# Optimization experiments

Measured on AMD Instinct MI355X. Metric: run time of the kernel, lower is better.

## Reference

```python
import jax, jax.numpy as jnp
import numpy as np

N_NODES = 10000
N_EDGES = 320000
IN_FEATS = 512
OUT_FEATS = 64


def gcn(feat, src, dst, W, b):
    """DGL GraphConv with norm='both', allow_zero_in_degree=True.
    out = D_in^{-1/2} * A^T * (D_out^{-1/2} * feat) @ W + b  (degrees clamped to >=1).
    """
    ones_e = jnp.ones(src.shape[0], dtype=feat.dtype)
    deg_out = jnp.clip(jax.ops.segment_sum(ones_e, src, num_segments=N_NODES), 1.0)
    deg_in = jnp.clip(jax.ops.segment_sum(ones_e, dst, num_segments=N_NODES), 1.0)
    h = feat * jax.lax.rsqrt(deg_out)[:, None]          # [N, F_in]
    h = h @ W                                            # [N, F_out] (project first, F_in >= F_out)
    agg = jax.ops.segment_sum(h[src], dst, num_segments=N_NODES)  # [N, F_out]
    return agg * jax.lax.rsqrt(deg_in)[:, None] + b


def setup_inputs() -> dict:
    key = jax.random.key(0)
    ks = jax.random.split(key, 8)
    feat = jax.random.normal(ks[0], (N_NODES, IN_FEATS), dtype=jnp.float32)
    eps = jax.random.normal(ks[1], (N_NODES, OUT_FEATS), dtype=jnp.float32)
    src = jax.random.randint(ks[2], (N_EDGES,), 0, N_NODES, dtype=jnp.int32)
    dst = jax.random.randint(ks[3], (N_EDGES,), 0, N_NODES, dtype=jnp.int32)
    s1 = 1.0 / np.sqrt(IN_FEATS)
    s2 = 1.0 / np.sqrt(OUT_FEATS)
    W1 = jax.random.normal(ks[4], (IN_FEATS, OUT_FEATS), dtype=jnp.float32) * s1
    Wmu = jax.random.normal(ks[5], (OUT_FEATS, OUT_FEATS), dtype=jnp.float32) * s2
    Wstd = jax.random.normal(ks[6], (OUT_FEATS, OUT_FEATS), dtype=jnp.float32) * s2 - 2.0 * s2
    b1 = jnp.zeros((OUT_FEATS,), dtype=jnp.float32)
    bmu = jnp.zeros((OUT_FEATS,), dtype=jnp.float32)
    bstd = jnp.zeros((OUT_FEATS,), dtype=jnp.float32)
    return {"feat": feat, "eps": eps, "src": src, "dst": dst,
            "W1": W1, "b1": b1, "Wmu": Wmu, "bmu": bmu, "Wstd": Wstd, "bstd": bstd}


def reference(feat, eps, src, dst, W1, b1, Wmu, bmu, Wstd, bstd):
    h1 = gcn(feat, src, dst, W1, b1)            # [N, out]
    mu = gcn(h1, src, dst, Wmu, bmu)            # [N, out]
    logvar = gcn(h1, src, dst, Wstd, bstd)      # [N, out]
    std = jnp.exp(logvar)                       # logvar.exp_() is in-place in torch
    z = eps * std + mu                          # reparametrize
    adj = jax.nn.sigmoid(z @ z.T)               # [N, N] dense decode
    return adj, mu, std                         # torch returns mutated logvar (== std)
```

## Files before the change

### kernel.cpp

```cpp
#include <hip/hip_runtime.h>
#include <stdint.h>

#define N_NODES 10000
#define N_EDGES 320000
#define F_IN 512
#define F_OUT 64

typedef __attribute__((ext_vector_type(8)))  __bf16 bf16x8;
typedef __attribute__((ext_vector_type(8)))  short  short8;
typedef __attribute__((ext_vector_type(16))) float  f32x16;
typedef __attribute__((ext_vector_type(4)))  float  float4v;

#define OFF_H1P    0
#define OFF_H1     640000
#define OFF_MUP    1280000
#define OFF_STDP   1920000
#define OFF_DEGIN  2560000
#define OFF_DEGOUT 2570000
#define OFF_OFFS   2580000
#define OFF_CURS   2592000
#define OFF_SCIN   2604000
#define OFF_SCOUT  2616000
#define OFF_CSR    2628000
#define OFF_WBUF   2948000

__device__ __forceinline__ unsigned short f2bf(float f) {
    unsigned u = __builtin_bit_cast(unsigned, f);
    u += 0x7fffu + ((u >> 16) & 1u);
    return (unsigned short)(u >> 16);
}
__device__ __forceinline__ float bf2f(unsigned short h) {
    unsigned u = ((unsigned)h) << 16;
    return __builtin_bit_cast(float, u);
}
__device__ __forceinline__ f32x16 zero16() {
    f32x16 v;
#pragma unroll
    for (int i = 0; i < 16; ++i) v[i] = 0.f;
    return v;
}

__global__ void k0_deg_wswz(const int* __restrict__ src, const int* __restrict__ dst,
                            const float* __restrict__ W1,
                            int* __restrict__ deg_out, int* __restrict__ deg_in,
                            unsigned short* __restrict__ wbuf) {
    int bid = blockIdx.x, tid = threadIdx.x;
    if (bid < 1250) {
        int e = bid * 256 + tid;
        if (e < N_EDGES) {
            atomicAdd(&deg_out[src[e]], 1);
            atomicAdd(&deg_in[dst[e]], 1);
        }
    } else {
        int q = (bid - 1250) * 256 + tid;
        int j = q & 7, l = (q >> 3) & 63, c = (q >> 9) & 31, t = q >> 14;
        int k = c * 16 + ((l >> 5) << 3) + j;
        int n = (t << 5) + (l & 31);
        wbuf[q] = f2bf(W1[k * F_OUT + n]);
    }
}

__global__ void __launch_bounds__(1024) k1_scan(const int* __restrict__ deg_in,
                                                const int* __restrict__ deg_out,
                                                int* __restrict__ offs, int* __restrict__ curs,
                                                float* __restrict__ sc_in, float* __restrict__ sc_out) {
    __shared__ int sdata[1024];
    int t = threadIdx.x;
    int loc[10];
    int s = 0;
#pragma unroll
    for (int u = 0; u < 10; ++u) {
        int idx = t * 10 + u;
        int v = (idx < N_NODES) ? deg_in[idx] : 0;
        loc[u] = v; s += v;
    }
    sdata[t] = s;
    __syncthreads();
    for (int off = 1; off < 1024; off <<= 1) {
        int v = sdata[t];
        int add = (t >= off) ? sdata[t - off] : 0;
        __syncthreads();
        sdata[t] = v + add;
        __syncthreads();
    }
    int run = (t == 0) ? 0 : sdata[t - 1];
#pragma unroll
    for (int u = 0; u < 10; ++u) {
        int idx = t * 10 + u;
        if (idx < N_NODES) {
            offs[idx] = run; curs[idx] = run;
            run += loc[u];
            sc_in[idx] = rsqrtf((float)max(loc[u], 1));
            sc_out[idx] = rsqrtf((float)max(deg_out[idx], 1));
        }
    }
    if (t == 1023) offs[N_NODES] = sdata[1023];
}

__global__ void k2_csr(const int* __restrict__ src, const int* __restrict__ dst,
                       int* __restrict__ curs, int* __restrict__ csr) {
    int e = blockIdx.x * 256 + threadIdx.x;
    if (e < N_EDGES) {
        int d = dst[e];
        int p = atomicAdd(&curs[d], 1);
        csr[p] = src[e];
    }
}

__global__ void __launch_bounds__(256) k3_proj1(const float* __restrict__ feat,
                                                const unsigned short* __restrict__ wbuf,
                                                const float* __restrict__ sc_out,
                                                float* __restrict__ h1p) {
    __shared__ float red[4][32 * 64];
    int tid = threadIdx.x;
    int wid = tid >> 6;
    int l = tid & 63;
    int half = l >> 5;
    int rowbase = blockIdx.x * 32;
    int m = rowbase + (l & 31);
    if (m > N_NODES - 1) m = N_NODES - 1;
    const float* arow = feat + (size_t)m * F_IN + half * 8;

    f32x16 acc0 = zero16(), acc1 = zero16();
    int cbeg = wid * 8;
#pragma unroll
    for (int cc = 0; cc < 8; ++cc) {
        int c = cbeg + cc;
        float4v a0 = *(const float4v*)(arow + c * 16);
        float4v a1 = *(const float4v*)(arow + c * 16 + 4);
        short8 as;
        as[0] = (short)f2bf(a0[0]); as[1] = (short)f2bf(a0[1]);
        as[2] = (short)f2bf(a0[2]); as[3] = (short)f2bf(a0[3]);
        as[4] = (short)f2bf(a1[0]); as[5] = (short)f2bf(a1[1]);
        as[6] = (short)f2bf(a1[2]); as[7] = (short)f2bf(a1[3]);
        bf16x8 af = __builtin_bit_cast(bf16x8, as);
        bf16x8 b0 = __builtin_bit_cast(bf16x8, *(const short8*)(wbuf + (size_t)((0 * 32 + c) * 64 + l) * 8));
        bf16x8 b1 = __builtin_bit_cast(bf16x8, *(const short8*)(wbuf + (size_t)((1 * 32 + c) * 64 + l) * 8));
        acc0 = __builtin_amdgcn_mfma_f32_32x32x16_bf16(af, b0, acc0, 0, 0, 0);
        acc1 = __builtin_amdgcn_mfma_f32_32x32x16_bf16(af, b1, acc1, 0, 0, 0);
    }
#pragma unroll
    for (int r = 0; r < 16; ++r) {
        int row = (r & 3) + 8 * (r >> 2) + 4 * half;
        int col = l & 31;
        red[wid][row * 64 + col] = acc0[r];
        red[wid][row * 64 + 32 + col] = acc1[r];
    }
    __syncthreads();
#pragma unroll
    for (int i = 0; i < 8; ++i) {
        int idx = tid * 8 + i;
        int row = idx >> 6, col = idx & 63;
        int gr = rowbase + row;
        if (gr < N_NODES) {
            float v = red[0][idx] + red[1][idx] + red[2][idx] + red[3][idx];
            h1p[gr * F_OUT + col] = v * sc_out[gr];
        }
    }
}

__global__ void __launch_bounds__(256) k4_gather1(const int* __restrict__ offs, const int* __restrict__ csr,
                                                  const float* __restrict__ h1p, const float* __restrict__ sc_in,
                                                  const float* __restrict__ b1, float* __restrict__ h1) {
    int tid = threadIdx.x;
    int n = blockIdx.x * 4 + (tid >> 6);
    int o = tid & 63;
    int e0 = offs[n], e1 = offs[n + 1];
    float acc = 0.f;
    for (int e = e0; e < e1; ++e) {
        int s = csr[e];
        acc += h1p[s * F_OUT + o];
    }
    h1[n * F_OUT + o] = acc * sc_in[n] + b1[o];
}

__global__ void __launch_bounds__(256) k5_proj2(const float* __restrict__ h1,
                                                const float* __restrict__ Wmu, const float* __restrict__ Wstd,
                                                const float* __restrict__ sc_out,
                                                float* __restrict__ mup, float* __restrict__ stdp) {
    __shared__ float wmuT[64 * 65];
    __shared__ float wstdT[64 * 65];
    __shared__ float hrow[4 * 64];
    int tid = threadIdx.x;
    for (int i = tid; i < 4096; i += 256) {
        int k = i >> 6, o2 = i & 63;
        wmuT[o2 * 65 + k] = Wmu[i];
        wstdT[o2 * 65 + k] = Wstd[i];
    }
    int ln = tid >> 6, o = tid & 63;
    int n = blockIdx.x * 4 + ln;
    hrow[ln * 64 + o] = h1[n * F_OUT + o];
    __syncthreads();
    float amu = 0.f, asd = 0.f;
#pragma unroll
    for (int k = 0; k < 64; ++k) {
        float h = hrow[ln * 64 + k];
        amu += h * wmuT[o * 65 + k];
        asd += h * wstdT[o * 65 + k];
    }
    float s = sc_out[n];
    mup[n * F_OUT + o] = amu * s;
    stdp[n * F_OUT + o] = asd * s;
}

__global__ void __launch_bounds__(256) k6_gather2(const int* __restrict__ offs, const int* __restrict__ csr,
                                                  const float* __restrict__ mup, const float* __restrict__ stdp,
                                                  const float* __restrict__ sc_in,
                                                  const float* __restrict__ bmu, const float* __restrict__ bstd,
                                                  const float* __restrict__ eps,
                                                  float* __restrict__ out_mu, float* __restrict__ out_std,
                                                  unsigned short* __restrict__ zhi, unsigned short* __restrict__ zlo) {
    int tid = threadIdx.x;
    int n = blockIdx.x * 4 + (tid >> 6);
    int o = tid & 63;
    int e0 = offs[n], e1 = offs[n + 1];
    float amu = 0.f, alv = 0.f;
    for (int e = e0; e < e1; ++e) {
        int s = csr[e];
        amu += mup[s * F_OUT + o];
        alv += stdp[s * F_OUT + o];
    }
    float si = sc_in[n];
    float mu = amu * si + bmu[o];
    float lv = alv * si + bstd[o];
    float sd = __expf(lv);
    float z = eps[n * F_OUT + o] * sd + mu;
    out_mu[n * F_OUT + o] = mu;
    out_std[n * F_OUT + o] = sd;
    unsigned short h = f2bf(z);
    zhi[n * F_OUT + o] = h;
    zlo[n * F_OUT + o] = f2bf(z - bf2f(h));
}

#define NT_TILES 157
#define NT_CB    40
__global__ void __launch_bounds__(256) k7_adj(const unsigned short* __restrict__ zhi,
                                              const unsigned short* __restrict__ zlo,
                                              float* __restrict__ adj) {
    int bid = blockIdx.x;
    int xcd = bid & 7;
    int i = bid >> 3;
    int cb = i % NT_CB;
    int sti = xcd + 8 * (i / NT_CB);
    if (sti >= NT_TILES) return;

    int tid = threadIdx.x;
    int wid = tid >> 6, l = tid & 63;
    int stj = cb * 4 + wid;
    bool do_store = (stj < NT_TILES);
    if (stj >= NT_TILES) stj = NT_TILES - 1;

    int rbase = sti * 64, cbase = stj * 64;
    int half = l >> 5, lm = l & 31;
    int koff = half * 8;

    int ra0 = min(rbase + lm, N_NODES - 1);
    int ra1 = min(rbase + 32 + lm, N_NODES - 1);
    int rb0 = min(cbase + lm, N_NODES - 1);
    int rb1 = min(cbase + 32 + lm, N_NODES - 1);

    f32x16 acc[2][2];
    acc[0][0] = zero16(); acc[0][1] = zero16();
    acc[1][0] = zero16(); acc[1][1] = zero16();

#pragma unroll
    for (int c = 0; c < 4; ++c) {
        int ko = c * 16 + koff;
        bf16x8 ah[2], al[2], bh[2], bl[2];
        ah[0] = __builtin_bit_cast(bf16x8, *(const short8*)(zhi + (size_t)ra0 * 64 + ko));
        ah[1] = __builtin_bit_cast(bf16x8, *(const short8*)(zhi + (size_t)ra1 * 64 + ko));
        al[0] = __builtin_bit_cast(bf16x8, *(const short8*)(zlo + (size_t)ra0 * 64 + ko));
        al[1] = __builtin_bit_cast(bf16x8, *(const short8*)(zlo + (size_t)ra1 * 64 + ko));
        bh[0] = __builtin_bit_cast(bf16x8, *(const short8*)(zhi + (size_t)rb0 * 64 + ko));
        bh[1] = __builtin_bit_cast(bf16x8, *(const short8*)(zhi + (size_t)rb1 * 64 + ko));
        bl[0] = __builtin_bit_cast(bf16x8, *(const short8*)(zlo + (size_t)rb0 * 64 + ko));
        bl[1] = __builtin_bit_cast(bf16x8, *(const short8*)(zlo + (size_t)rb1 * 64 + ko));
#pragma unroll
        for (int rt = 0; rt < 2; ++rt)
#pragma unroll
            for (int ct = 0; ct < 2; ++ct) {
                acc[rt][ct] = __builtin_amdgcn_mfma_f32_32x32x16_bf16(ah[rt], bh[ct], acc[rt][ct], 0, 0, 0);
                acc[rt][ct] = __builtin_amdgcn_mfma_f32_32x32x16_bf16(ah[rt], bl[ct], acc[rt][ct], 0, 0, 0);
                acc[rt][ct] = __builtin_amdgcn_mfma_f32_32x32x16_bf16(al[rt], bh[ct], acc[rt][ct], 0, 0, 0);
            }
    }

#pragma unroll
    for (int rt = 0; rt < 2; ++rt)
#pragma unroll
        for (int ct = 0; ct < 2; ++ct) {
#pragma unroll
            for (int r = 0; r < 16; ++r) {
                int row = rbase + rt * 32 + (r & 3) + 8 * (r >> 2) + 4 * half;
                int col = cbase + ct * 32 + lm;
                if (do_store && row < N_NODES && col < N_NODES) {
                    float x = acc[rt][ct][r];
                    float sig = 1.f / (1.f + __expf(-x));
                    __builtin_nontemporal_store(sig, &adj[(long)row * N_NODES + col]);
                }
            }
        }
}

extern "C" void kernel_launch(void* const* d_in, const int* in_sizes, int n_in,
                              void* d_out, int out_size, void* d_ws, size_t ws_size,
                              hipStream_t stream) {
    const float* feat = (const float*)d_in[0];
    const float* eps  = (const float*)d_in[1];
    const int*   src  = (const int*)d_in[2];
    const int*   dst  = (const int*)d_in[3];
    const float* W1   = (const float*)d_in[4];
    const float* b1   = (const float*)d_in[5];
    const float* Wmu  = (const float*)d_in[6];
    const float* bmu  = (const float*)d_in[7];
    const float* Wstd = (const float*)d_in[8];
    const float* bstd = (const float*)d_in[9];

    float* out = (float*)d_out;
    float* adj     = out;
    float* out_mu  = out + 100000000;
    float* out_std = out_mu + 640000;

    float* h1p  = out + OFF_H1P;
    float* h1   = out + OFF_H1;
    float* mup  = out + OFF_MUP;
    float* stdp = out + OFF_STDP;
    int* deg_in  = (int*)(out + OFF_DEGIN);
    int* deg_out = (int*)(out + OFF_DEGOUT);
    int* offs    = (int*)(out + OFF_OFFS);
    int* curs    = (int*)(out + OFF_CURS);
    float* sc_in  = out + OFF_SCIN;
    float* sc_out = out + OFF_SCOUT;
    int* csr = (int*)(out + OFF_CSR);
    unsigned short* wbuf = (unsigned short*)(out + OFF_WBUF);

    unsigned short* zhi = (unsigned short*)d_ws;
    unsigned short* zlo = zhi + 640000;

    hipMemsetAsync(out + OFF_DEGIN, 0, 20000 * sizeof(int), stream);

    k0_deg_wswz<<<1378, 256, 0, stream>>>(src, dst, W1, deg_out, deg_in, wbuf);
    k1_scan<<<1, 1024, 0, stream>>>(deg_in, deg_out, offs, curs, sc_in, sc_out);
    k2_csr<<<1250, 256, 0, stream>>>(src, dst, curs, csr);
    k3_proj1<<<313, 256, 0, stream>>>(feat, wbuf, sc_out, h1p);
    k4_gather1<<<2500, 256, 0, stream>>>(offs, csr, h1p, sc_in, b1, h1);
    k5_proj2<<<2500, 256, 0, stream>>>(h1, Wmu, Wstd, sc_out, mup, stdp);
    k6_gather2<<<2500, 256, 0, stream>>>(offs, csr, mup, stdp, sc_in, bmu, bstd, eps,
                                         out_mu, out_std, zhi, zlo);
    k7_adj<<<8 * 20 * NT_CB, 256, 0, stream>>>(zhi, zlo, adj);
}
```

Before: 631.9 us.

## Fuse gather1 with proj2, unroll gathers, stage adj tiles in LDS for vector stores

Merges the first aggregation and the mu/std projection into one 1024-thread kernel, so the h1 intermediate is no longer written and read back from global memory. That fused kernel and the second gather unroll their edge loops by four to keep more independent loads in flight. The dense decode kernel now writes sigmoid results into a shared-memory tile and emits coalesced float4 nontemporal stores instead of scattered scalar stores. The cost is extra LDS use and two barriers per row half in the adj kernel, plus lower occupancy from the 1024-thread blocks.

```diff
diff --git a/kernel.cpp b/kernel.cpp
--- a/kernel.cpp
+++ b/kernel.cpp
@@ -159,37 +159,39 @@
     }
 }
 
-__global__ void __launch_bounds__(256) k4_gather1(const int* __restrict__ offs, const int* __restrict__ csr,
-                                                  const float* __restrict__ h1p, const float* __restrict__ sc_in,
-                                                  const float* __restrict__ b1, float* __restrict__ h1) {
-    int tid = threadIdx.x;
-    int n = blockIdx.x * 4 + (tid >> 6);
-    int o = tid & 63;
-    int e0 = offs[n], e1 = offs[n + 1];
-    float acc = 0.f;
-    for (int e = e0; e < e1; ++e) {
-        int s = csr[e];
-        acc += h1p[s * F_OUT + o];
-    }
-    h1[n * F_OUT + o] = acc * sc_in[n] + b1[o];
-}
-
-__global__ void __launch_bounds__(256) k5_proj2(const float* __restrict__ h1,
-                                                const float* __restrict__ Wmu, const float* __restrict__ Wstd,
-                                                const float* __restrict__ sc_out,
-                                                float* __restrict__ mup, float* __restrict__ stdp) {
+__global__ void __launch_bounds__(1024) k45_gather_proj(
+        const int* __restrict__ offs, const int* __restrict__ csr,
+        const float* __restrict__ h1p,
+        const float* __restrict__ sc_in, const float* __restrict__ sc_out,
+        const float* __restrict__ b1,
+        const float* __restrict__ Wmu, const float* __restrict__ Wstd,
+        float* __restrict__ mup, float* __restrict__ stdp) {
     __shared__ float wmuT[64 * 65];
     __shared__ float wstdT[64 * 65];
-    __shared__ float hrow[4 * 64];
+    __shared__ float hrow[16 * 64];
     int tid = threadIdx.x;
-    for (int i = tid; i < 4096; i += 256) {
+#pragma unroll
+    for (int i0 = 0; i0 < 4096; i0 += 1024) {
+        int i = i0 + tid;
         int k = i >> 6, o2 = i & 63;
         wmuT[o2 * 65 + k] = Wmu[i];
         wstdT[o2 * 65 + k] = Wstd[i];
     }
     int ln = tid >> 6, o = tid & 63;
-    int n = blockIdx.x * 4 + ln;
-    hrow[ln * 64 + o] = h1[n * F_OUT + o];
+    int n = blockIdx.x * 16 + ln;
+    int e0 = offs[n], e1 = offs[n + 1];
+    float acc = 0.f;
+    int e = e0;
+    for (; e + 4 <= e1; e += 4) {
+        int s0 = csr[e], s1 = csr[e + 1], s2 = csr[e + 2], s3 = csr[e + 3];
+        float v0 = h1p[s0 * F_OUT + o];
+        float v1 = h1p[s1 * F_OUT + o];
+        float v2 = h1p[s2 * F_OUT + o];
+        float v3 = h1p[s3 * F_OUT + o];
+        acc += v0; acc += v1; acc += v2; acc += v3;
+    }
+    for (; e < e1; ++e) acc += h1p[csr[e] * F_OUT + o];
+    hrow[ln * 64 + o] = acc * sc_in[n] + b1[o];
     __syncthreads();
     float amu = 0.f, asd = 0.f;
 #pragma unroll
@@ -215,7 +217,17 @@
     int o = tid & 63;
     int e0 = offs[n], e1 = offs[n + 1];
     float amu = 0.f, alv = 0.f;
-    for (int e = e0; e < e1; ++e) {
+    int e = e0;
+    for (; e + 4 <= e1; e += 4) {
+        int s0 = csr[e], s1 = csr[e + 1], s2 = csr[e + 2], s3 = csr[e + 3];
+        float m0 = mup[s0 * F_OUT + o], l0 = stdp[s0 * F_OUT + o];
+        float m1 = mup[s1 * F_OUT + o], l1 = stdp[s1 * F_OUT + o];
+        float m2 = mup[s2 * F_OUT + o], l2 = stdp[s2 * F_OUT + o];
+        float m3 = mup[s3 * F_OUT + o], l3 = stdp[s3 * F_OUT + o];
+        amu += m0; amu += m1; amu += m2; amu += m3;
+        alv += l0; alv += l1; alv += l2; alv += l3;
+    }
+    for (; e < e1; ++e) {
         int s = csr[e];
         amu += mup[s * F_OUT + o];
         alv += stdp[s * F_OUT + o];
@@ -237,6 +249,7 @@
 __global__ void __launch_bounds__(256) k7_adj(const unsigned short* __restrict__ zhi,
                                               const unsigned short* __restrict__ zlo,
                                               float* __restrict__ adj) {
+    __shared__ float red[32 * 256];
     int bid = blockIdx.x;
     int xcd = bid & 7;
     int i = bid >> 3;
@@ -247,10 +260,9 @@
     int tid = threadIdx.x;
     int wid = tid >> 6, l = tid & 63;
     int stj = cb * 4 + wid;
-    bool do_store = (stj < NT_TILES);
-    if (stj >= NT_TILES) stj = NT_TILES - 1;
-
-    int rbase = sti * 64, cbase = stj * 64;
+    int stjc = min(stj, NT_TILES - 1);
+
+    int rbase = sti * 64, cbase = stjc * 64;
     int half = l >> 5, lm = l & 31;
     int koff = half * 8;
 
@@ -285,21 +297,34 @@
             }
     }
 
-#pragma unroll
-    for (int rt = 0; rt < 2; ++rt)
-#pragma unroll
-        for (int ct = 0; ct < 2; ++ct) {
+    int colOrigin = cb * 256;
+#pragma unroll
+    for (int rt = 0; rt < 2; ++rt) {
+#pragma unroll
+        for (int ct = 0; ct < 2; ++ct)
 #pragma unroll
             for (int r = 0; r < 16; ++r) {
-                int row = rbase + rt * 32 + (r & 3) + 8 * (r >> 2) + 4 * half;
-                int col = cbase + ct * 32 + lm;
-                if (do_store && row < N_NODES && col < N_NODES) {
-                    float x = acc[rt][ct][r];
-                    float sig = 1.f / (1.f + __expf(-x));
-                    __builtin_nontemporal_store(sig, &adj[(long)row * N_NODES + col]);
-                }
+                int row = (r & 3) + 8 * (r >> 2) + 4 * half;
+                int col = wid * 64 + ct * 32 + lm;
+                float x = acc[rt][ct][r];
+                float sig = __builtin_amdgcn_rcpf(1.f + __expf(-x));
+                red[row * 256 + col] = sig;
+            }
+        __syncthreads();
+#pragma unroll
+        for (int it = 0; it < 8; ++it) {
+            int fid = it * 256 + tid;
+            int row = fid >> 6;
+            int c4 = (fid & 63) * 4;
+            int grow = rbase + rt * 32 + row;
+            int gcol = colOrigin + c4;
+            if (grow < N_NODES && gcol < N_NODES) {
+                float4v v = *(const float4v*)&red[row * 256 + c4];
+                __builtin_nontemporal_store(v, (float4v*)&adj[(size_t)grow * N_NODES + gcol]);
             }
         }
+        __syncthreads();
+    }
 }
 
 extern "C" void kernel_launch(void* const* d_in, const int* in_sizes, int n_in,
@@ -322,7 +347,6 @@
     float* out_std = out_mu + 640000;
 
     float* h1p  = out + OFF_H1P;
-    float* h1   = out + OFF_H1;
     float* mup  = out + OFF_MUP;
     float* stdp = out + OFF_STDP;
     int* deg_in  = (int*)(out + OFF_DEGIN);
@@ -343,8 +367,8 @@
     k1_scan<<<1, 1024, 0, stream>>>(deg_in, deg_out, offs, curs, sc_in, sc_out);
     k2_csr<<<1250, 256, 0, stream>>>(src, dst, curs, csr);
     k3_proj1<<<313, 256, 0, stream>>>(feat, wbuf, sc_out, h1p);
-    k4_gather1<<<2500, 256, 0, stream>>>(offs, csr, h1p, sc_in, b1, h1);
-    k5_proj2<<<2500, 256, 0, stream>>>(h1, Wmu, Wstd, sc_out, mup, stdp);
+    k45_gather_proj<<<625, 1024, 0, stream>>>(offs, csr, h1p, sc_in, sc_out, b1,
+                                              Wmu, Wstd, mup, stdp);
     k6_gather2<<<2500, 256, 0, stream>>>(offs, csr, mup, stdp, sc_in, bmu, bstd, eps,
                                          out_mu, out_std, zhi, zlo);
     k7_adj<<<8 * 20 * NT_CB, 256, 0, stream>>>(zhi, zlo, adj);
```

Result: faster. 585.5 us (-7.4%).
